# Kernel optimization log

Measured on AMD Instinct MI355X. Metric: run time of the kernel, lower is better.

The kernel has to match this reference:

```python
import jax, jax.numpy as jnp
import numpy as np

N_NODES = 100000
N_EDGES = 1600000


def gcn_conv(x, edge_index, W, b, num_nodes):
    # PyG GCNConv: add self-loops, symmetric deg^-1/2 normalization, linear, scatter-add, bias
    h = x @ W  # [N, out]
    loop = jnp.arange(num_nodes)
    row = jnp.concatenate([edge_index[0], loop])
    col = jnp.concatenate([edge_index[1], loop])
    deg = jax.ops.segment_sum(jnp.ones_like(col, dtype=h.dtype), col, num_segments=num_nodes)
    dinv = jnp.where(deg > 0, deg ** -0.5, 0.0)
    norm = dinv[row] * dinv[col]  # [E+N]
    msg = h[row] * norm[:, None]  # gather + scale
    out = jax.ops.segment_sum(msg, col, num_segments=num_nodes)
    return out + b


def setup_inputs() -> dict:
    key = jax.random.key(0)
    ks = jax.random.split(key, 12)
    x = jax.random.normal(ks[0], (N_NODES, 2), dtype=jnp.float32)
    edge_index = jax.random.randint(ks[1], (2, N_EDGES), 0, N_NODES, dtype=jnp.int64)
    edge_attr = jax.random.uniform(ks[2], (N_EDGES, 1), dtype=jnp.float32)
    W1 = jax.random.normal(ks[3], (2, 64), dtype=jnp.float32) * 0.5
    b1 = jnp.zeros((64,), dtype=jnp.float32)
    W2 = jax.random.normal(ks[4], (64, 32), dtype=jnp.float32) * (64 ** -0.5)
    b2 = jnp.zeros((32,), dtype=jnp.float32)
    mW1 = jax.random.normal(ks[5], (65, 16), dtype=jnp.float32) * (65 ** -0.5)
    mb1 = jnp.zeros((16,), dtype=jnp.float32)
    mW2 = jax.random.normal(ks[6], (16, 1), dtype=jnp.float32) * (16 ** -0.5)
    mb2 = jnp.zeros((1,), dtype=jnp.float32)
    return {"x": x, "edge_index": edge_index, "edge_attr": edge_attr,
            "num_nodes": N_NODES,
            "W1": W1, "b1": b1, "W2": W2, "b2": b2,
            "mW1": mW1, "mb1": mb1, "mW2": mW2, "mb2": mb2}


def reference(x, edge_index, edge_attr, num_nodes, W1, b1, W2, b2, mW1, mb1, mW2, mb2):
    h = jax.nn.relu(gcn_conv(x, edge_index, W1, b1, num_nodes))
    h = jax.nn.relu(gcn_conv(h, edge_index, W2, b2, num_nodes))
    row, col = edge_index[0], edge_index[1]
    ef = jnp.concatenate([h[row], h[col], edge_attr], axis=1)  # [E, 65]
    hid = jax.nn.relu(ef @ mW1 + mb1)
    return jax.nn.sigmoid(hid @ mW2 + mb2)  # [E, 1]
```

## Files before the change

kernel.cpp:

```cpp
#include <hip/hip_runtime.h>
#include <hip/hip_fp16.h>
#include <math.h>


__global__ void k_count(const int* __restrict__ col, int* __restrict__ deg, int E) {
    int stride = gridDim.x * blockDim.x;
    for (int e = blockIdx.x * blockDim.x + threadIdx.x; e < E; e += stride)
        atomicAdd(deg + col[e], 1);
}

__global__ void k_scan1(const int* __restrict__ deg, int* __restrict__ start,
                        int* __restrict__ bsum, int N) {
    __shared__ int sd[256];
    int t = threadIdx.x;
    int n = blockIdx.x * 256 + t;
    int d = (n < N) ? deg[n] : 0;
    sd[t] = d;
    __syncthreads();
    for (int off = 1; off < 256; off <<= 1) {
        int tv = (t >= off) ? sd[t - off] : 0;
        __syncthreads();
        sd[t] += tv;
        __syncthreads();
    }
    if (n < N) start[n] = sd[t] - d;
    if (t == 255) bsum[blockIdx.x] = sd[255];
}

__global__ void k_scan2(int* __restrict__ bsum, int nb) {
    __shared__ int sd[512];
    int t = threadIdx.x;
    int d = (t < nb) ? bsum[t] : 0;
    sd[t] = d;
    __syncthreads();
    for (int off = 1; off < 512; off <<= 1) {
        int tv = (t >= off) ? sd[t - off] : 0;
        __syncthreads();
        sd[t] += tv;
        __syncthreads();
    }
    if (t < nb) bsum[t] = sd[t] - d;
}

__global__ void k_scan3(int* __restrict__ start, const int* __restrict__ bsum,
                        int* __restrict__ cursor, const int* __restrict__ deg,
                        const float* __restrict__ x, float* __restrict__ dinv,
                        float* __restrict__ xs, int N) {
    int n = blockIdx.x * 256 + threadIdx.x;
    if (n >= N) return;
    int s = start[n] + bsum[blockIdx.x];
    start[n] = s;
    cursor[n] = s;
    float di = rsqrtf((float)deg[n] + 1.0f);
    dinv[n] = di;
    xs[2 * n] = x[2 * n] * di;
    xs[2 * n + 1] = x[2 * n + 1] * di;
}

__global__ void k_fill(const int* __restrict__ row, const int* __restrict__ col,
                       int* __restrict__ cursor, int* __restrict__ srcidx,
                       int E, int wshift, int nph) {
    int g      = blockIdx.x & 7;
    int tid0   = (blockIdx.x >> 3) * blockDim.x + threadIdx.x;
    int stride = (gridDim.x >> 3) * blockDim.x;
    for (int ph = g; ph < nph; ph += 8) {
        for (int e = tid0; e < E; e += stride) {
            int c = col[e];
            if ((c >> wshift) == ph) {
                int p = atomicAdd(cursor + c, 1);
                srcidx[p] = row[e];
            }
        }
    }
}

__global__ void k_l1l2(const int* __restrict__ start, const int* __restrict__ deg,
                       const int* __restrict__ srcidx,
                       const float* __restrict__ xs, const float* __restrict__ dinv,
                       const float* __restrict__ W1, const float* __restrict__ b1,
                       const float* __restrict__ W2,
                       __half* __restrict__ hs2h, int N) {
    __shared__ float sW1[128], sb1[64], sW2[2048];
    for (int i = threadIdx.x; i < 128;  i += blockDim.x) sW1[i] = W1[i];
    for (int i = threadIdx.x; i < 64;   i += blockDim.x) sb1[i] = b1[i];
    for (int i = threadIdx.x; i < 2048; i += blockDim.x) sW2[i] = W2[i];
    __syncthreads();
    int n = blockIdx.x * 256 + threadIdx.x;
    if (n >= N) return;
    int s = start[n], cnt = deg[n];
    float a0 = xs[2 * n], a1 = xs[2 * n + 1];
    for (int k = 0; k < cnt; ++k) {
        int r = srcidx[s + k];
        a0 += xs[2 * r];
        a1 += xs[2 * r + 1];
    }
    float di = dinv[n];
    a0 *= di; a1 *= di;
    float acc[32];
#pragma unroll
    for (int j = 0; j < 32; ++j) acc[j] = 0.0f;
    for (int k = 0; k < 64; ++k) {
        float h = fmaxf(fmaf(a0, sW1[k], fmaf(a1, sW1[64 + k], sb1[k])), 0.0f);
#pragma unroll
        for (int j = 0; j < 32; ++j) acc[j] = fmaf(h, sW2[k * 32 + j], acc[j]);
    }
    __half2 hb[16];
#pragma unroll
    for (int j = 0; j < 16; ++j)
        hb[j] = __floats2half2_rn(acc[2 * j] * di, acc[2 * j + 1] * di);
    float4* op = (float4*)(hs2h + (size_t)n * 32);
    const float4* ip = (const float4*)hb;
#pragma unroll
    for (int q = 0; q < 4; ++q) op[q] = ip[q];
}

__global__ void k_agg2uv(const int* __restrict__ start, const int* __restrict__ deg,
                         const int* __restrict__ srcidx,
                         const __half* __restrict__ hs2h, const float* __restrict__ dinv,
                         const float* __restrict__ b2, const float* __restrict__ mW1,
                         __half* __restrict__ u16, __half* __restrict__ v16, int N) {
    __shared__ float sA[512], sB[512], sb2[32];
    __shared__ float h2s[8][32];
    for (int i = threadIdx.x; i < 512; i += 256) { sA[i] = mW1[i]; sB[i] = mW1[512 + i]; }
    if (threadIdx.x < 32) sb2[threadIdx.x] = b2[threadIdx.x];
    __syncthreads();
    int g  = threadIdx.x >> 5;
    int ch = threadIdx.x & 31;
    int n  = blockIdx.x * 8 + g;
    if (n < N) {
        int s = start[n], cnt = deg[n];
        float acc = __half2float(hs2h[(size_t)n * 32 + ch]);
        for (int k = 0; k < cnt; ++k) {
            int r = srcidx[s + k];
            acc += __half2float(hs2h[(size_t)r * 32 + ch]);
        }
        h2s[g][ch] = fmaxf(fmaf(acc, dinv[n], sb2[ch]), 0.0f);
    }
    __syncthreads();
    if (n >= N) return;
    const float* M = (ch < 16) ? sA : sB;
    int i = ch & 15;
    float s0 = 0.0f;
#pragma unroll
    for (int j = 0; j < 32; ++j) s0 = fmaf(h2s[g][j], M[j * 16 + i], s0);
    if (ch < 16) u16[(size_t)n * 16 + i] = __float2half_rn(s0);
    else         v16[(size_t)n * 16 + i] = __float2half_rn(s0);
}

__device__ inline void unpack8(const float4 f, float* o) {
    const __half2* h2 = (const __half2*)&f;
#pragma unroll
    for (int i = 0; i < 4; ++i) {
        float2 t = __half22float2(h2[i]);
        o[2 * i] = t.x; o[2 * i + 1] = t.y;
    }
}

__global__ void k_edge(const int* __restrict__ row, const int* __restrict__ col,
                       const float* __restrict__ ea,
                       const __half* __restrict__ u16, const __half* __restrict__ v16,
                       const float* __restrict__ mW1, const float* __restrict__ mb1,
                       const float* __restrict__ mW2, const float* __restrict__ mb2,
                       float* __restrict__ out, int E) {
    __shared__ float sC[16], sb1[16], sW2v[16], sb2s;
    if (threadIdx.x < 16) {
        sC[threadIdx.x]   = mW1[64 * 16 + threadIdx.x];
        sb1[threadIdx.x]  = mb1[threadIdx.x];
        sW2v[threadIdx.x] = mW2[threadIdx.x];
    }
    if (threadIdx.x == 0) sb2s = mb2[0];
    __syncthreads();
    int tid    = blockIdx.x * blockDim.x + threadIdx.x;
    int stride = gridDim.x * blockDim.x;
    for (int e0 = tid * 2; e0 < E; e0 += stride * 2) {
        int e1 = e0 + 1;
        bool two = (e1 < E);
        int2 r2 = *(const int2*)(row + e0);
        int2 c2 = *(const int2*)(col + e0);
        float2 a2 = *(const float2*)(ea + e0);
        const float4* up0 = (const float4*)(u16 + (size_t)r2.x * 16);
        const float4* vp0 = (const float4*)(v16 + (size_t)c2.x * 16);
        const float4* up1 = (const float4*)(u16 + (size_t)r2.y * 16);
        const float4* vp1 = (const float4*)(v16 + (size_t)c2.y * 16);
        float4 ua0 = up0[0], ub0 = up0[1];
        float4 va0 = vp0[0], vb0 = vp0[1];
        float4 ua1 = up1[0], ub1 = up1[1];
        float4 va1 = vp1[0], vb1 = vp1[1];
        float uf0[16], vf0[16], uf1[16], vf1[16];
        unpack8(ua0, uf0); unpack8(ub0, uf0 + 8);
        unpack8(va0, vf0); unpack8(vb0, vf0 + 8);
        unpack8(ua1, uf1); unpack8(ub1, uf1 + 8);
        unpack8(va1, vf1); unpack8(vb1, vf1 + 8);
        float s0 = sb2s, s1 = sb2s;
#pragma unroll
        for (int i = 0; i < 16; ++i) {
            float t0 = fmaf(a2.x, sC[i], sb1[i]);
            float t1 = fmaf(a2.y, sC[i], sb1[i]);
            float h0 = fmaxf(uf0[i] + vf0[i] + t0, 0.0f);
            float h1 = fmaxf(uf1[i] + vf1[i] + t1, 0.0f);
            s0 = fmaf(h0, sW2v[i], s0);
            s1 = fmaf(h1, sW2v[i], s1);
        }
        float o0 = 1.0f / (1.0f + expf(-s0));
        float o1 = 1.0f / (1.0f + expf(-s1));
        if (two) {
            *(float2*)(out + e0) = make_float2(o0, o1);
        } else {
            out[e0] = o0;
        }
    }
}

extern "C" void kernel_launch(void* const* d_in, const int* in_sizes, int n_in,
                              void* d_out, int out_size, void* d_ws, size_t ws_size,
                              hipStream_t stream) {
    const float* x   = (const float*)d_in[0];
    const int*   ei  = (const int*)d_in[1];
    const float* ea  = (const float*)d_in[2];
    const float* W1  = (const float*)d_in[4];
    const float* b1  = (const float*)d_in[5];
    const float* W2  = (const float*)d_in[6];
    const float* b2  = (const float*)d_in[7];
    const float* mW1 = (const float*)d_in[8];
    const float* mb1 = (const float*)d_in[9];
    const float* mW2 = (const float*)d_in[10];
    const float* mb2 = (const float*)d_in[11];
    float* out = (float*)d_out;

    int N = in_sizes[0] / 2;
    int E = in_sizes[2];
    const int* row = ei;
    const int* col = ei + E;

    int clog = 0; while ((1u << clog) < (unsigned)N) ++clog;
    int wshift = clog > 3 ? clog - 3 : 0;
    int nph = ((N - 1) >> wshift) + 1;

    int* deg    = (int*)d_ws;
    int* start  = deg + N;
    int* cursor = start + N;
    int* bsum   = cursor + N;
    int* srcidx = bsum + 1024;
    float* dinv = (float*)(srcidx + E);
    float* xs   = dinv + (size_t)N;
    __half* hs2h = (__half*)(xs + (size_t)2 * N);
    __half* u16  = hs2h + (size_t)32 * N;
    __half* v16  = u16 + (size_t)16 * N;

    int nb_n = (N + 255) / 256;

    hipMemsetAsync(deg, 0, (size_t)N * sizeof(int), stream);
    k_count<<<2048, 256, 0, stream>>>(col, deg, E);
    k_scan1<<<nb_n, 256, 0, stream>>>(deg, start, bsum, N);
    k_scan2<<<1, 512, 0, stream>>>(bsum, nb_n);
    k_scan3<<<nb_n, 256, 0, stream>>>(start, bsum, cursor, deg, x, dinv, xs, N);
    k_fill <<<2048, 256, 0, stream>>>(row, col, cursor, srcidx, E, wshift, nph);
    k_l1l2 <<<nb_n, 256, 0, stream>>>(start, deg, srcidx, xs, dinv, W1, b1, W2, hs2h, N);
    k_agg2uv<<<(N + 7) / 8, 256, 0, stream>>>(start, deg, srcidx, hs2h, dinv, b2, mW1, u16, v16, N);
    k_edge <<<2048, 256, 0, stream>>>(row, col, ea, u16, v16, mW1, mb1, mW2, mb2, out, E);
}
```

Measured before the change: 390.3 us.

## Use full 64-lane wavefront per node in layer-2 aggregation with shuffle-based projection

Reworks k_agg2uv so each node is handled by a full 64-lane wavefront instead of a 32-thread half. The two halves split the neighbor list, and each half keeps two accumulators to raise memory-level parallelism. The halves are combined with a cross-half shuffle, and the 32x32 projection into u/v is done with register shuffles instead of shared memory and __syncthreads. This aims to hide gather latency and remove the block barrier, at the cost of twice as many blocks and idle lanes in the final stores.

```diff
diff --git a/kernel.cpp b/kernel.cpp
--- a/kernel.cpp
+++ b/kernel.cpp
@@ -120,31 +120,55 @@
                          const float* __restrict__ b2, const float* __restrict__ mW1,
                          __half* __restrict__ u16, __half* __restrict__ v16, int N) {
     __shared__ float sA[512], sB[512], sb2[32];
-    __shared__ float h2s[8][32];
     for (int i = threadIdx.x; i < 512; i += 256) { sA[i] = mW1[i]; sB[i] = mW1[512 + i]; }
     if (threadIdx.x < 32) sb2[threadIdx.x] = b2[threadIdx.x];
     __syncthreads();
-    int g  = threadIdx.x >> 5;
-    int ch = threadIdx.x & 31;
-    int n  = blockIdx.x * 8 + g;
-    if (n < N) {
-        int s = start[n], cnt = deg[n];
-        float acc = __half2float(hs2h[(size_t)n * 32 + ch]);
-        for (int k = 0; k < cnt; ++k) {
-            int r = srcidx[s + k];
-            acc += __half2float(hs2h[(size_t)r * 32 + ch]);
-        }
-        h2s[g][ch] = fmaxf(fmaf(acc, dinv[n], sb2[ch]), 0.0f);
-    }
-    __syncthreads();
+    int L  = threadIdx.x & 63;
+    int w  = threadIdx.x >> 6;
+    int ch = L & 31;
+    int h  = L >> 5;
+    int n  = blockIdx.x * 4 + w;
     if (n >= N) return;
-    const float* M = (ch < 16) ? sA : sB;
-    int i = ch & 15;
-    float s0 = 0.0f;
-#pragma unroll
-    for (int j = 0; j < 32; ++j) s0 = fmaf(h2s[g][j], M[j * 16 + i], s0);
-    if (ch < 16) u16[(size_t)n * 16 + i] = __float2half_rn(s0);
-    else         v16[(size_t)n * 16 + i] = __float2half_rn(s0);
+
+    int s = start[n], cnt = deg[n];
+    float acc0 = (h == 0) ? __half2float(hs2h[(size_t)n * 32 + ch]) : 0.0f;
+    float acc1 = 0.0f;
+    int k = 0;
+    for (; k + 3 < cnt; k += 4) {
+        int ra = srcidx[s + k + h];
+        int rb = srcidx[s + k + 2 + h];
+        acc0 += __half2float(hs2h[(size_t)ra * 32 + ch]);
+        acc1 += __half2float(hs2h[(size_t)rb * 32 + ch]);
+    }
+    for (; k + 1 < cnt; k += 2) {
+        int r = srcidx[s + k + h];
+        acc0 += __half2float(hs2h[(size_t)r * 32 + ch]);
+    }
+    if (k < cnt && h == 0) {
+        int r = srcidx[s + k];
+        acc0 += __half2float(hs2h[(size_t)r * 32 + ch]);
+    }
+    float acc = acc0 + acc1;
+    acc += __shfl_xor(acc, 32);
+    float h2 = fmaxf(fmaf(acc, dinv[n], sb2[ch]), 0.0f);
+
+    int jh = L >> 5;
+    int os = (L >> 4) & 1;
+    int i  = L & 15;
+    const float* M = os ? sB : sA;
+    float part = 0.0f;
+#pragma unroll
+    for (int t = 0; t < 16; ++t) {
+        int j = jh * 16 + t;
+        float hj = __shfl(h2, j);
+        part = fmaf(hj, M[j * 16 + i], part);
+    }
+    part += __shfl_xor(part, 32);
+    if (L < 32) {
+        __half val = __float2half_rn(part);
+        if (os == 0) u16[(size_t)n * 16 + i] = val;
+        else         v16[(size_t)n * 16 + i] = val;
+    }
 }
 
 __device__ inline void unpack8(const float4 f, float* o) {
@@ -256,6 +280,6 @@
     k_scan3<<<nb_n, 256, 0, stream>>>(start, bsum, cursor, deg, x, dinv, xs, N);
     k_fill <<<2048, 256, 0, stream>>>(row, col, cursor, srcidx, E, wshift, nph);
     k_l1l2 <<<nb_n, 256, 0, stream>>>(start, deg, srcidx, xs, dinv, W1, b1, W2, hs2h, N);
-    k_agg2uv<<<(N + 7) / 8, 256, 0, stream>>>(start, deg, srcidx, hs2h, dinv, b2, mW1, u16, v16, N);
+    k_agg2uv<<<(N + 3) / 4, 256, 0, stream>>>(start, deg, srcidx, hs2h, dinv, b2, mW1, u16, v16, N);
     k_edge <<<2048, 256, 0, stream>>>(row, col, ea, u16, v16, mW1, mb1, mW2, mb2, out, E);
 }
```

Result: faster. 365.8 us (-6.3%).
